# Optimization experiments

Measured on AMD Instinct MI355X. Metric: run time of the kernel, lower is better.

## Reference

```python
import jax, jax.numpy as jnp
import numpy as np

S, R, C, H, D = 128, 384, 256, 8, 32  # N_seq, N_res, C_m, heads, head_dim
INF = 1e9
EPS = 1e-5


def _layernorm(x, w, b):
    mu = jnp.mean(x, axis=-1, keepdims=True)
    var = jnp.mean(jnp.square(x - mu), axis=-1, keepdims=True)
    return (x - mu) * jax.lax.rsqrt(var + EPS) * w + b


def setup_inputs() -> dict:
    key = jax.random.key(0)
    ks = jax.random.split(key, 8)
    sc = 0.02
    m = jax.random.normal(ks[0], (S, R, C), jnp.float32)
    mask = jnp.ones((S, R), jnp.float32)
    ln_w = jnp.ones((C,), jnp.float32)
    ln_b = jnp.zeros((C,), jnp.float32)
    wq = jax.random.normal(ks[1], (C, H * D), jnp.float32) * sc
    wk = jax.random.normal(ks[2], (C, H * D), jnp.float32) * sc
    wv = jax.random.normal(ks[3], (C, H * D), jnp.float32) * sc
    wg = jax.random.normal(ks[4], (C, H * D), jnp.float32) * sc
    bg = jnp.ones((H * D,), jnp.float32)  # gate bias init to 1 (openfold convention)
    wo = jax.random.normal(ks[5], (H * D, C), jnp.float32) * sc
    bo = jnp.zeros((C,), jnp.float32)
    return {"m": m, "mask": mask, "ln_w": ln_w, "ln_b": ln_b,
            "wq": wq, "wk": wk, "wv": wv, "wg": wg, "bg": bg,
            "wo": wo, "bo": bo}


def reference(m, mask, ln_w, ln_b, wq, wk, wv, wg, bg, wo, bo):
    # mask bias: [S, 1, 1, R], 0 where mask==1, -inf-ish where mask==0
    mask_bias = (INF * (mask - 1.0))[:, None, None, :]
    x = _layernorm(m, ln_w, ln_b)                        # [S, R, C]
    q = (x @ wq).reshape(S, R, H, D) * (D ** -0.5)       # [S, R, H, D]
    k = (x @ wk).reshape(S, R, H, D)
    v = (x @ wv).reshape(S, R, H, D)
    scores = jnp.einsum('sqhd,skhd->shqk', q, k) + mask_bias  # [S, H, R, R]
    a = jax.nn.softmax(scores, axis=-1)
    o = jnp.einsum('shqk,skhd->sqhd', a, v)              # [S, R, H, D]
    g = jax.nn.sigmoid(x @ wg + bg).reshape(S, R, H, D)  # gate
    o = (o * g).reshape(S, R, H * D)
    return o @ wo + bo                                   # [S, R, C]
```

## Files before the change

kernel.cpp:

```cpp
#include <hip/hip_runtime.h>
#include <cstdint>
#include <cstddef>

#define S_  128
#define R_  384
#define C_  256
#define H_  8
#define D_  32
#define HD_ 256
#define M_  (S_*R_)

typedef float f32x16 __attribute__((ext_vector_type(16)));
typedef short s16x8  __attribute__((ext_vector_type(8)));
typedef int   i32x4  __attribute__((ext_vector_type(4)));

__device__ __forceinline__ unsigned short f2bf(float f) {
  uint32_t u = __float_as_uint(f);
  u += 0x7fffu + ((u >> 16) & 1u);
  return (unsigned short)(u >> 16);
}
__device__ __forceinline__ float bf2f(unsigned short s) {
  return __uint_as_float(((uint32_t)s) << 16);
}
__device__ __forceinline__ uint32_t pkbf(float lo, float hi) {
  return (uint32_t)f2bf(lo) | ((uint32_t)f2bf(hi) << 16);
}
#define MFMA32(a,b,c) __builtin_amdgcn_mfma_f32_32x32x16_bf16((a),(b),(c),0,0,0)

__global__ __launch_bounds__(256) void prep_w(const float* __restrict__ wq,
    const float* __restrict__ wk, const float* __restrict__ wv,
    const float* __restrict__ wg, const float* __restrict__ wo,
    unsigned short* __restrict__ WT) {
  int idx = blockIdx.x * 256 + threadIdx.x;
  int mat = idx >> 16;
  int rem = idx & 65535;
  int n = rem >> 8, k = rem & 255;
  const float* W = (mat==0)?wq:(mat==1)?wk:(mat==2)?wv:(mat==3)?wg:wo;
  WT[idx] = f2bf(W[k*256 + n]);
}

__global__ __launch_bounds__(256) void ln_kernel(const float* __restrict__ mIn,
    const float* __restrict__ w, const float* __restrict__ b,
    unsigned short* __restrict__ x) {
  int row  = blockIdx.x * 4 + (threadIdx.x >> 6);
  int lane = threadIdx.x & 63;
  const float4 v4 = *(const float4*)(mIn + (size_t)row * C_ + lane * 4);
  float s  = v4.x + v4.y + v4.z + v4.w;
  float ss = v4.x*v4.x + v4.y*v4.y + v4.z*v4.z + v4.w*v4.w;
#pragma unroll
  for (int off = 32; off > 0; off >>= 1) {
    s  += __shfl_xor(s,  off);
    ss += __shfl_xor(ss, off);
  }
  float mu  = s * (1.0f / C_);
  float var = ss * (1.0f / C_) - mu * mu;
  float rs  = rsqrtf(var + 1e-5f);
  const float4 wv = *(const float4*)(w + lane * 4);
  const float4 bv = *(const float4*)(b + lane * 4);
  uint2 o2;
  o2.x = pkbf((v4.x - mu) * rs * wv.x + bv.x, (v4.y - mu) * rs * wv.y + bv.y);
  o2.y = pkbf((v4.z - mu) * rs * wv.z + bv.z, (v4.w - mu) * rs * wv.w + bv.w);
  *(uint2*)(x + (size_t)row * C_ + lane * 4) = o2;
}

__global__ __launch_bounds__(256) void proj_gemm(const unsigned short* __restrict__ X,
    const unsigned short* __restrict__ WT, const float* __restrict__ bg,
    unsigned short* __restrict__ Qo, unsigned short* __restrict__ Ko,
    unsigned short* __restrict__ Vo, unsigned short* __restrict__ Go) {
  __shared__ unsigned short As[128][40];
  __shared__ unsigned short Bs[128][40];
  const int tid = threadIdx.x;
  const int bm  = blockIdx.x * 128;
  const int wi  = blockIdx.y >> 1;
  const int bn  = (blockIdx.y & 1) * 128;
  const unsigned short* Wt = WT + wi * 65536;
  unsigned short* O = (wi==0)?Qo:(wi==1)?Ko:(wi==2)?Vo:Go;

  const int lane = tid & 63, wid = tid >> 6;
  const int wm = (wid >> 1) * 64, wn = (wid & 1) * 64;
  const int lr = lane & 31, hi = lane >> 5;
  const int sr = tid >> 1, sc = (tid & 1) * 16;

  f32x16 acc[2][2];
#pragma unroll
  for (int i = 0; i < 2; i++)
#pragma unroll
    for (int j = 0; j < 2; j++)
#pragma unroll
      for (int r = 0; r < 16; r++) acc[i][j][r] = 0.f;

  for (int k0 = 0; k0 < 256; k0 += 32) {
    const uint4* xs = (const uint4*)(X + (size_t)(bm + sr) * 256 + k0 + sc);
    uint4 x0 = xs[0], x1 = xs[1];
    const uint4* wsrc = (const uint4*)(Wt + (size_t)(bn + sr) * 256 + k0 + sc);
    uint4 b0 = wsrc[0], b1 = wsrc[1];
    *(uint4*)&As[sr][sc] = x0; *(uint4*)&As[sr][sc + 8] = x1;
    *(uint4*)&Bs[sr][sc] = b0; *(uint4*)&Bs[sr][sc + 8] = b1;
    __syncthreads();
#pragma unroll
    for (int kh = 0; kh < 2; kh++) {
      s16x8 a0  = *(const s16x8*)&As[wm + lr][kh*16 + 8*hi];
      s16x8 a1  = *(const s16x8*)&As[wm + 32 + lr][kh*16 + 8*hi];
      s16x8 bb0 = *(const s16x8*)&Bs[wn + lr][kh*16 + 8*hi];
      s16x8 bb1 = *(const s16x8*)&Bs[wn + 32 + lr][kh*16 + 8*hi];
      acc[0][0] = MFMA32(a0, bb0, acc[0][0]);
      acc[0][1] = MFMA32(a0, bb1, acc[0][1]);
      acc[1][0] = MFMA32(a1, bb0, acc[1][0]);
      acc[1][1] = MFMA32(a1, bb1, acc[1][1]);
    }
    __syncthreads();
  }

  const float qs = 0.17677669529663687f;
#pragma unroll
  for (int ms = 0; ms < 2; ms++) {
#pragma unroll
    for (int ns = 0; ns < 2; ns++) {
      int colg = bn + wn + ns*32 + lr;
      float bgv = (wi == 3) ? bg[colg] : 0.f;
#pragma unroll
      for (int r = 0; r < 16; r++) {
        float v = acc[ms][ns][r];
        if (wi == 0) v *= qs;
        if (wi == 3) v = 1.0f / (1.0f + __expf(-(v + bgv)));
        int row = bm + wm + ms*32 + (r & 3) + 8*(r >> 2) + 4*hi;
        O[(size_t)row * 256 + colg] = f2bf(v);
      }
    }
  }
}

__global__ __launch_bounds__(256) void attn_kernel(const unsigned short* __restrict__ Qb,
    const unsigned short* __restrict__ Kb, const unsigned short* __restrict__ Vb,
    const float* __restrict__ mask, unsigned short* __restrict__ Ob) {
  __shared__ unsigned short Kl[384][40];
  __shared__ unsigned short VT[32][392];
  __shared__ float mb[384];
  __shared__ float sAl[4][32];

  const int h = blockIdx.x, s = blockIdx.y;
  const int tid = threadIdx.x;
  const int lane = tid & 63, wid = tid >> 6;
  const int lr = lane & 31, hi = lane >> 5;

#pragma unroll
  for (int i = 0; i < 3; i++) {
    int rh = tid + 256*i;
    int r = rh >> 1, c0 = (rh & 1) * 16;
    const unsigned short* ksrc = Kb + ((size_t)(s*R_ + r)) * 256 + h*32 + c0;
    *(uint4*)&Kl[r][c0]     = *(const uint4*)ksrc;
    *(uint4*)&Kl[r][c0 + 8] = *(const uint4*)(ksrc + 8);
    const unsigned short* vsrc = Vb + ((size_t)(s*R_ + r)) * 256 + h*32 + c0;
    unsigned short tmp[16];
    *(uint4*)tmp       = *(const uint4*)vsrc;
    *(uint4*)(tmp + 8) = *(const uint4*)(vsrc + 8);
#pragma unroll
    for (int j = 0; j < 16; j++) VT[c0 + j][r] = tmp[j];
  }
  for (int r = tid; r < 384; r += 256) mb[r] = 1e9f * (mask[s*R_ + r] - 1.0f);

  s16x8 bq[3][2];
#pragma unroll
  for (int st = 0; st < 3; st++)
#pragma unroll
    for (int kh = 0; kh < 2; kh++)
      bq[st][kh] = *(const s16x8*)(Qb + ((size_t)(s*R_ + wid*96 + st*32 + lr)) * 256
                                   + h*32 + kh*16 + 8*hi);

  f32x16 of[3];
#pragma unroll
  for (int st = 0; st < 3; st++)
#pragma unroll
    for (int r = 0; r < 16; r++) of[st][r] = 0.f;
  float mrun[3] = {-1e30f, -1e30f, -1e30f};
  float lsum[3] = {0.f, 0.f, 0.f};

  __syncthreads();

  for (int kt = 0; kt < 12; kt++) {
    s16x8 ak0 = *(const s16x8*)&Kl[kt*32 + lr][8*hi];
    s16x8 ak1 = *(const s16x8*)&Kl[kt*32 + lr][16 + 8*hi];
    s16x8 bv0 = *(const s16x8*)&VT[lr][kt*32 + 8*hi];
    s16x8 bv1 = *(const s16x8*)&VT[lr][kt*32 + 16 + 8*hi];
    float mbr[16];
#pragma unroll
    for (int r = 0; r < 16; r++) mbr[r] = mb[kt*32 + (r & 3) + 8*(r >> 2) + 4*hi];

#pragma unroll
    for (int st = 0; st < 3; st++) {
      f32x16 p;
#pragma unroll
      for (int r = 0; r < 16; r++) p[r] = 0.f;
      p = MFMA32(ak0, bq[st][0], p);
      p = MFMA32(ak1, bq[st][1], p);
      float pm = -1e30f;
#pragma unroll
      for (int r = 0; r < 16; r++) { p[r] += mbr[r]; pm = fmaxf(pm, p[r]); }
      pm = fmaxf(pm, __shfl_xor(pm, 32));
      if (!__all(pm <= mrun[st] + 8.0f)) {
        float nm = fmaxf(mrun[st], pm);
        float al = __expf(mrun[st] - nm);
        mrun[st] = nm;
        lsum[st] *= al;
        if (hi == 0) sAl[wid][lr] = al;
        float alr[16];
#pragma unroll
        for (int r = 0; r < 16; r++) alr[r] = sAl[wid][(r & 3) + 8*(r >> 2) + 4*hi];
#pragma unroll
        for (int r = 0; r < 16; r++) of[st][r] *= alr[r];
      }
      float ls = 0.f;
#pragma unroll
      for (int r = 0; r < 16; r++) { p[r] = __expf(p[r] - mrun[st]); ls += p[r]; }
      lsum[st] += ls;
      uint32_t w0 = pkbf(p[0],  p[1]),  w1 = pkbf(p[2],  p[3]);
      uint32_t w2 = pkbf(p[4],  p[5]),  w3 = pkbf(p[6],  p[7]);
      uint32_t w4 = pkbf(p[8],  p[9]),  w5 = pkbf(p[10], p[11]);
      uint32_t w6 = pkbf(p[12], p[13]), w7 = pkbf(p[14], p[15]);
      asm volatile("v_permlane32_swap_b32 %0, %1" : "+v"(w0), "+v"(w2));
      asm volatile("v_permlane32_swap_b32 %0, %1" : "+v"(w1), "+v"(w3));
      asm volatile("v_permlane32_swap_b32 %0, %1" : "+v"(w4), "+v"(w6));
      asm volatile("v_permlane32_swap_b32 %0, %1" : "+v"(w5), "+v"(w7));
      i32x4 pa0i = {(int)w0, (int)w1, (int)w2, (int)w3};
      i32x4 pa1i = {(int)w4, (int)w5, (int)w6, (int)w7};
      of[st] = MFMA32(__builtin_bit_cast(s16x8, pa0i), bv0, of[st]);
      of[st] = MFMA32(__builtin_bit_cast(s16x8, pa1i), bv1, of[st]);
    }
  }

#pragma unroll
  for (int st = 0; st < 3; st++) {
    float lt = lsum[st] + __shfl_xor(lsum[st], 32);
    float inv = 1.0f / lt;
    if (hi == 0) sAl[wid][lr] = inv;
    float ivr[16];
#pragma unroll
    for (int r = 0; r < 16; r++) ivr[r] = sAl[wid][(r & 3) + 8*(r >> 2) + 4*hi];
#pragma unroll
    for (int r = 0; r < 16; r++) {
      int row = wid*96 + st*32 + (r & 3) + 8*(r >> 2) + 4*hi;
      Ob[((size_t)(s*R_ + row)) * 256 + h*32 + lr] = f2bf(of[st][r] * ivr[r]);
    }
  }
}

__global__ __launch_bounds__(256) void out_gemm(const unsigned short* __restrict__ Ob,
    const unsigned short* __restrict__ Gb, const unsigned short* __restrict__ WT,
    const float* __restrict__ bo, float* __restrict__ Out) {
  __shared__ unsigned short As[128][40];
  __shared__ unsigned short Bs[128][40];
  const unsigned short* Wt = WT + 4 * 65536;
  const int tid = threadIdx.x;
  const int bm = blockIdx.x * 128;
  const int bn = blockIdx.y * 128;
  const int lane = tid & 63, wid = tid >> 6;
  const int wm = (wid >> 1) * 64, wn = (wid & 1) * 64;
  const int lr = lane & 31, hi = lane >> 5;
  const int sr = tid >> 1, sc = (tid & 1) * 16;

  f32x16 acc[2][2];
#pragma unroll
  for (int i = 0; i < 2; i++)
#pragma unroll
    for (int j = 0; j < 2; j++)
#pragma unroll
      for (int r = 0; r < 16; r++) acc[i][j][r] = 0.f;

  for (int k0 = 0; k0 < 256; k0 += 32) {
    const unsigned short* orow = Ob + (size_t)(bm + sr) * 256 + k0 + sc;
    const unsigned short* grow = Gb + (size_t)(bm + sr) * 256 + k0 + sc;
    unsigned short ot[16], gt[16], res[16];
    *(uint4*)ot       = *(const uint4*)orow;
    *(uint4*)(ot + 8) = *(const uint4*)(orow + 8);
    *(uint4*)gt       = *(const uint4*)grow;
    *(uint4*)(gt + 8) = *(const uint4*)(grow + 8);
#pragma unroll
    for (int j = 0; j < 16; j++) res[j] = f2bf(bf2f(ot[j]) * bf2f(gt[j]));
    const uint4* wsrc = (const uint4*)(Wt + (size_t)(bn + sr) * 256 + k0 + sc);
    uint4 b0 = wsrc[0], b1 = wsrc[1];
    *(uint4*)&As[sr][sc] = *(uint4*)res; *(uint4*)&As[sr][sc + 8] = *(uint4*)(res + 8);
    *(uint4*)&Bs[sr][sc] = b0;           *(uint4*)&Bs[sr][sc + 8] = b1;
    __syncthreads();
#pragma unroll
    for (int kh = 0; kh < 2; kh++) {
      s16x8 a0  = *(const s16x8*)&As[wm + lr][kh*16 + 8*hi];
      s16x8 a1  = *(const s16x8*)&As[wm + 32 + lr][kh*16 + 8*hi];
      s16x8 bb0 = *(const s16x8*)&Bs[wn + lr][kh*16 + 8*hi];
      s16x8 bb1 = *(const s16x8*)&Bs[wn + 32 + lr][kh*16 + 8*hi];
      acc[0][0] = MFMA32(a0, bb0, acc[0][0]);
      acc[0][1] = MFMA32(a0, bb1, acc[0][1]);
      acc[1][0] = MFMA32(a1, bb0, acc[1][0]);
      acc[1][1] = MFMA32(a1, bb1, acc[1][1]);
    }
    __syncthreads();
  }

#pragma unroll
  for (int ms = 0; ms < 2; ms++) {
#pragma unroll
    for (int ns = 0; ns < 2; ns++) {
      int colg = bn + wn + ns*32 + lr;
      float bov = bo[colg];
#pragma unroll
      for (int r = 0; r < 16; r++) {
        int row = bm + wm + ms*32 + (r & 3) + 8*(r >> 2) + 4*hi;
        Out[(size_t)row * 256 + colg] = acc[ms][ns][r] + bov;
      }
    }
  }
}

extern "C" void kernel_launch(void* const* d_in, const int* in_sizes, int n_in,
                              void* d_out, int out_size, void* d_ws, size_t ws_size,
                              hipStream_t stream) {
  const float* m    = (const float*)d_in[0];
  const float* mask = (const float*)d_in[1];
  const float* ln_w = (const float*)d_in[2];
  const float* ln_b = (const float*)d_in[3];
  const float* wq   = (const float*)d_in[4];
  const float* wk   = (const float*)d_in[5];
  const float* wv   = (const float*)d_in[6];
  const float* wg   = (const float*)d_in[7];
  const float* bg   = (const float*)d_in[8];
  const float* wo   = (const float*)d_in[9];
  const float* bo   = (const float*)d_in[10];
  float* out = (float*)d_out;

  unsigned short* ws = (unsigned short*)d_ws;
  const size_t SZ = (size_t)M_ * 256;
  unsigned short* xbf = ws;
  unsigned short* qb  = ws + 1 * SZ;
  unsigned short* kb  = ws + 2 * SZ;
  unsigned short* vb  = ws + 3 * SZ;
  unsigned short* gb  = ws + 4 * SZ;
  unsigned short* ob  = ws + 5 * SZ;
  unsigned short* WT  = ws + 6 * SZ;

  prep_w<<<1280, 256, 0, stream>>>(wq, wk, wv, wg, wo, WT);
  ln_kernel<<<M_ / 4, 256, 0, stream>>>(m, ln_w, ln_b, xbf);
  proj_gemm<<<dim3(M_ / 128, 8), 256, 0, stream>>>(xbf, WT, bg, qb, kb, vb, gb);
  attn_kernel<<<dim3(H_, S_), 256, 0, stream>>>(qb, kb, vb, mask, ob);
  out_gemm<<<dim3(M_ / 128, 2), 256, 0, stream>>>(ob, gb, WT, bo, out);
}
```

Baseline: 270.5 us.

## Use direct global-to-LDS loads, exp2 softmax, gate fusion into attention, tiled weight transpose

The weight-prep kernel now transposes through shared-memory tiles so that both its reads and writes are coalesced. Both GEMMs stage tiles with global_load_lds into unpadded LDS instead of going through registers. Attention folds log2(e) into the Q scale and the mask so the softmax can use exp2. It also loads K/V in two halves to cut LDS use, raises MFMA priority with setprio, and applies the sigmoid gate in its epilogue, so out_gemm no longer reads the gate tensor. The unpadded LDS layout may cause bank conflicts on the MFMA fragment reads.

Result: faster. 262.3 us (-3.0%).

```diff
diff --git a/kernel.cpp b/kernel.cpp
--- a/kernel.cpp
+++ b/kernel.cpp
@@ -10,6 +10,8 @@
 #define HD_ 256
 #define M_  (S_*R_)
 
+#define LOG2E 1.4426950408889634f
+
 typedef float f32x16 __attribute__((ext_vector_type(16)));
 typedef short s16x8  __attribute__((ext_vector_type(8)));
 typedef int   i32x4  __attribute__((ext_vector_type(4)));
@@ -27,16 +29,33 @@
 }
 #define MFMA32(a,b,c) __builtin_amdgcn_mfma_f32_32x32x16_bf16((a),(b),(c),0,0,0)
 
+__device__ __forceinline__ void gload16(const void* g, void* l) {
+  __builtin_amdgcn_global_load_lds(
+      (const __attribute__((address_space(1))) void*)g,
+      (__attribute__((address_space(3))) void*)l, 16, 0, 0);
+}
+
 __global__ __launch_bounds__(256) void prep_w(const float* __restrict__ wq,
     const float* __restrict__ wk, const float* __restrict__ wv,
     const float* __restrict__ wg, const float* __restrict__ wo,
     unsigned short* __restrict__ WT) {
-  int idx = blockIdx.x * 256 + threadIdx.x;
-  int mat = idx >> 16;
-  int rem = idx & 65535;
-  int n = rem >> 8, k = rem & 255;
+  __shared__ unsigned short Tl[64][72];
+  const int mat = blockIdx.x >> 4;
+  const int t   = blockIdx.x & 15;
+  const int k0  = (t >> 2) * 64, n0 = (t & 3) * 64;
   const float* W = (mat==0)?wq:(mat==1)?wk:(mat==2)?wv:(mat==3)?wg:wo;
-  WT[idx] = f2bf(W[k*256 + n]);
+  const int tx = threadIdx.x & 63, ty = threadIdx.x >> 6;
+#pragma unroll
+  for (int i = 0; i < 16; i++) {
+    int kk = ty + i * 4;
+    Tl[tx][kk] = f2bf(W[(size_t)(k0 + kk) * 256 + n0 + tx]);
+  }
+  __syncthreads();
+#pragma unroll
+  for (int i = 0; i < 16; i++) {
+    int nn = ty + i * 4;
+    WT[(size_t)mat * 65536 + (size_t)(n0 + nn) * 256 + k0 + tx] = Tl[nn][tx];
+  }
 }
 
 __global__ __launch_bounds__(256) void ln_kernel(const float* __restrict__ mIn,
@@ -67,19 +86,19 @@
     const unsigned short* __restrict__ WT, const float* __restrict__ bg,
     unsigned short* __restrict__ Qo, unsigned short* __restrict__ Ko,
     unsigned short* __restrict__ Vo, unsigned short* __restrict__ Go) {
-  __shared__ unsigned short As[128][40];
-  __shared__ unsigned short Bs[128][40];
+  __shared__ __align__(16) unsigned short As[128 * 32];
+  __shared__ __align__(16) unsigned short Bs[128 * 32];
   const int tid = threadIdx.x;
   const int bm  = blockIdx.x * 128;
   const int wi  = blockIdx.y >> 1;
   const int bn  = (blockIdx.y & 1) * 128;
-  const unsigned short* Wt = WT + wi * 65536;
+  const unsigned short* Wt = WT + (size_t)wi * 65536;
   unsigned short* O = (wi==0)?Qo:(wi==1)?Ko:(wi==2)?Vo:Go;
 
   const int lane = tid & 63, wid = tid >> 6;
   const int wm = (wid >> 1) * 64, wn = (wid & 1) * 64;
   const int lr = lane & 31, hi = lane >> 5;
-  const int sr = tid >> 1, sc = (tid & 1) * 16;
+  const int srow = lane >> 2, scol = (lane & 3) * 8;
 
   f32x16 acc[2][2];
 #pragma unroll
@@ -90,28 +109,29 @@
       for (int r = 0; r < 16; r++) acc[i][j][r] = 0.f;
 
   for (int k0 = 0; k0 < 256; k0 += 32) {
-    const uint4* xs = (const uint4*)(X + (size_t)(bm + sr) * 256 + k0 + sc);
-    uint4 x0 = xs[0], x1 = xs[1];
-    const uint4* wsrc = (const uint4*)(Wt + (size_t)(bn + sr) * 256 + k0 + sc);
-    uint4 b0 = wsrc[0], b1 = wsrc[1];
-    *(uint4*)&As[sr][sc] = x0; *(uint4*)&As[sr][sc + 8] = x1;
-    *(uint4*)&Bs[sr][sc] = b0; *(uint4*)&Bs[sr][sc + 8] = b1;
+#pragma unroll
+    for (int i = 0; i < 2; i++) {
+      const int rbase = wid * 32 + i * 16;
+      gload16(X  + (size_t)(bm + rbase + srow) * 256 + k0 + scol, &As[rbase * 32]);
+      gload16(Wt + (size_t)(bn + rbase + srow) * 256 + k0 + scol, &Bs[rbase * 32]);
+    }
+    asm volatile("s_waitcnt vmcnt(0)" ::: "memory");
     __syncthreads();
 #pragma unroll
     for (int kh = 0; kh < 2; kh++) {
-      s16x8 a0  = *(const s16x8*)&As[wm + lr][kh*16 + 8*hi];
-      s16x8 a1  = *(const s16x8*)&As[wm + 32 + lr][kh*16 + 8*hi];
-      s16x8 bb0 = *(const s16x8*)&Bs[wn + lr][kh*16 + 8*hi];
-      s16x8 bb1 = *(const s16x8*)&Bs[wn + 32 + lr][kh*16 + 8*hi];
-      acc[0][0] = MFMA32(a0, bb0, acc[0][0]);
-      acc[0][1] = MFMA32(a0, bb1, acc[0][1]);
-      acc[1][0] = MFMA32(a1, bb0, acc[1][0]);
-      acc[1][1] = MFMA32(a1, bb1, acc[1][1]);
-    }
-    __syncthreads();
-  }
-
-  const float qs = 0.17677669529663687f;
+      s16x8 a0 = *(const s16x8*)&As[(wm + lr) * 32      + kh*16 + 8*hi];
+      s16x8 a1 = *(const s16x8*)&As[(wm + 32 + lr) * 32 + kh*16 + 8*hi];
+      s16x8 b0 = *(const s16x8*)&Bs[(wn + lr) * 32      + kh*16 + 8*hi];
+      s16x8 b1 = *(const s16x8*)&Bs[(wn + 32 + lr) * 32 + kh*16 + 8*hi];
+      acc[0][0] = MFMA32(a0, b0, acc[0][0]);
+      acc[0][1] = MFMA32(a0, b1, acc[0][1]);
+      acc[1][0] = MFMA32(a1, b0, acc[1][0]);
+      acc[1][1] = MFMA32(a1, b1, acc[1][1]);
+    }
+    __syncthreads();
+  }
+
+  const float qs2 = 0.17677669529663687f * LOG2E;
 #pragma unroll
   for (int ms = 0; ms < 2; ms++) {
 #pragma unroll
@@ -121,7 +141,7 @@
 #pragma unroll
       for (int r = 0; r < 16; r++) {
         float v = acc[ms][ns][r];
-        if (wi == 0) v *= qs;
+        if (wi == 0) v *= qs2;
         if (wi == 3) v = 1.0f / (1.0f + __expf(-(v + bgv)));
         int row = bm + wm + ms*32 + (r & 3) + 8*(r >> 2) + 4*hi;
         O[(size_t)row * 256 + colg] = f2bf(v);
@@ -132,32 +152,21 @@
 
 __global__ __launch_bounds__(256) void attn_kernel(const unsigned short* __restrict__ Qb,
     const unsigned short* __restrict__ Kb, const unsigned short* __restrict__ Vb,
-    const float* __restrict__ mask, unsigned short* __restrict__ Ob) {
-  __shared__ unsigned short Kl[384][40];
-  __shared__ unsigned short VT[32][392];
+    const unsigned short* __restrict__ Gb, const float* __restrict__ mask,
+    unsigned short* __restrict__ Ob) {
+  __shared__ unsigned short Kl[192][40];
+  __shared__ unsigned short VT[32][200];
   __shared__ float mb[384];
   __shared__ float sAl[4][32];
 
   const int h = blockIdx.x, s = blockIdx.y;
   const int tid = threadIdx.x;
-  const int lane = tid & 63, wid = tid >> 6;
+  const int wid = tid >> 6;
+  const int lane = tid & 63;
   const int lr = lane & 31, hi = lane >> 5;
 
-#pragma unroll
-  for (int i = 0; i < 3; i++) {
-    int rh = tid + 256*i;
-    int r = rh >> 1, c0 = (rh & 1) * 16;
-    const unsigned short* ksrc = Kb + ((size_t)(s*R_ + r)) * 256 + h*32 + c0;
-    *(uint4*)&Kl[r][c0]     = *(const uint4*)ksrc;
-    *(uint4*)&Kl[r][c0 + 8] = *(const uint4*)(ksrc + 8);
-    const unsigned short* vsrc = Vb + ((size_t)(s*R_ + r)) * 256 + h*32 + c0;
-    unsigned short tmp[16];
-    *(uint4*)tmp       = *(const uint4*)vsrc;
-    *(uint4*)(tmp + 8) = *(const uint4*)(vsrc + 8);
-#pragma unroll
-    for (int j = 0; j < 16; j++) VT[c0 + j][r] = tmp[j];
-  }
-  for (int r = tid; r < 384; r += 256) mb[r] = 1e9f * (mask[s*R_ + r] - 1.0f);
+  for (int r = tid; r < 384; r += 256)
+    mb[r] = (1e9f * LOG2E) * (mask[s * R_ + r] - 1.0f);
 
   s16x8 bq[3][2];
 #pragma unroll
@@ -175,56 +184,86 @@
   float mrun[3] = {-1e30f, -1e30f, -1e30f};
   float lsum[3] = {0.f, 0.f, 0.f};
 
-  __syncthreads();
-
-  for (int kt = 0; kt < 12; kt++) {
-    s16x8 ak0 = *(const s16x8*)&Kl[kt*32 + lr][8*hi];
-    s16x8 ak1 = *(const s16x8*)&Kl[kt*32 + lr][16 + 8*hi];
-    s16x8 bv0 = *(const s16x8*)&VT[lr][kt*32 + 8*hi];
-    s16x8 bv1 = *(const s16x8*)&VT[lr][kt*32 + 16 + 8*hi];
-    float mbr[16];
-#pragma unroll
-    for (int r = 0; r < 16; r++) mbr[r] = mb[kt*32 + (r & 3) + 8*(r >> 2) + 4*hi];
-
-#pragma unroll
-    for (int st = 0; st < 3; st++) {
-      f32x16 p;
-#pragma unroll
-      for (int r = 0; r < 16; r++) p[r] = 0.f;
-      p = MFMA32(ak0, bq[st][0], p);
-      p = MFMA32(ak1, bq[st][1], p);
-      float pm = -1e30f;
-#pragma unroll
-      for (int r = 0; r < 16; r++) { p[r] += mbr[r]; pm = fmaxf(pm, p[r]); }
-      pm = fmaxf(pm, __shfl_xor(pm, 32));
-      if (!__all(pm <= mrun[st] + 8.0f)) {
-        float nm = fmaxf(mrun[st], pm);
-        float al = __expf(mrun[st] - nm);
-        mrun[st] = nm;
-        lsum[st] *= al;
-        if (hi == 0) sAl[wid][lr] = al;
-        float alr[16];
-#pragma unroll
-        for (int r = 0; r < 16; r++) alr[r] = sAl[wid][(r & 3) + 8*(r >> 2) + 4*hi];
-#pragma unroll
-        for (int r = 0; r < 16; r++) of[st][r] *= alr[r];
+  for (int ph = 0; ph < 2; ph++) {
+    __syncthreads();
+#pragma unroll
+    for (int i = 0; i < 2; i++) {
+      int rh = tid + 256 * i;
+      if (rh < 384) {
+        int rl = rh >> 1, c0 = (rh & 1) * 16;
+        int rg = ph * 192 + rl;
+        const unsigned short* ksrc = Kb + ((size_t)(s*R_ + rg)) * 256 + h*32 + c0;
+        *(uint4*)&Kl[rl][c0]     = *(const uint4*)ksrc;
+        *(uint4*)&Kl[rl][c0 + 8] = *(const uint4*)(ksrc + 8);
+        const unsigned short* vsrc = Vb + ((size_t)(s*R_ + rg)) * 256 + h*32 + c0;
+        unsigned short tmp[16];
+        *(uint4*)tmp       = *(const uint4*)vsrc;
+        *(uint4*)(tmp + 8) = *(const uint4*)(vsrc + 8);
+#pragma unroll
+        for (int j = 0; j < 16; j++) VT[c0 + j][rl] = tmp[j];
       }
-      float ls = 0.f;
-#pragma unroll
-      for (int r = 0; r < 16; r++) { p[r] = __expf(p[r] - mrun[st]); ls += p[r]; }
-      lsum[st] += ls;
-      uint32_t w0 = pkbf(p[0],  p[1]),  w1 = pkbf(p[2],  p[3]);
-      uint32_t w2 = pkbf(p[4],  p[5]),  w3 = pkbf(p[6],  p[7]);
-      uint32_t w4 = pkbf(p[8],  p[9]),  w5 = pkbf(p[10], p[11]);
-      uint32_t w6 = pkbf(p[12], p[13]), w7 = pkbf(p[14], p[15]);
-      asm volatile("v_permlane32_swap_b32 %0, %1" : "+v"(w0), "+v"(w2));
-      asm volatile("v_permlane32_swap_b32 %0, %1" : "+v"(w1), "+v"(w3));
-      asm volatile("v_permlane32_swap_b32 %0, %1" : "+v"(w4), "+v"(w6));
-      asm volatile("v_permlane32_swap_b32 %0, %1" : "+v"(w5), "+v"(w7));
-      i32x4 pa0i = {(int)w0, (int)w1, (int)w2, (int)w3};
-      i32x4 pa1i = {(int)w4, (int)w5, (int)w6, (int)w7};
-      of[st] = MFMA32(__builtin_bit_cast(s16x8, pa0i), bv0, of[st]);
-      of[st] = MFMA32(__builtin_bit_cast(s16x8, pa1i), bv1, of[st]);
+    }
+    __syncthreads();
+
+    for (int kt = 0; kt < 6; kt++) {
+      const int ktg = ph * 6 + kt;
+      s16x8 ak0 = *(const s16x8*)&Kl[kt*32 + lr][8*hi];
+      s16x8 ak1 = *(const s16x8*)&Kl[kt*32 + lr][16 + 8*hi];
+      s16x8 bv0 = *(const s16x8*)&VT[lr][kt*32 + 8*hi];
+      s16x8 bv1 = *(const s16x8*)&VT[lr][kt*32 + 16 + 8*hi];
+      float mbr[16];
+#pragma unroll
+      for (int r = 0; r < 16; r++) mbr[r] = mb[ktg*32 + (r & 3) + 8*(r >> 2) + 4*hi];
+
+#pragma unroll
+      for (int st = 0; st < 3; st++) {
+        f32x16 p;
+#pragma unroll
+        for (int r = 0; r < 16; r++) p[r] = mbr[r];
+        __builtin_amdgcn_s_setprio(1);
+        p = MFMA32(ak0, bq[st][0], p);
+        p = MFMA32(ak1, bq[st][1], p);
+        __builtin_amdgcn_s_setprio(0);
+        float m01 = fmaxf(fmaxf(p[0], p[1]), fmaxf(p[2], p[3]));
+        float m23 = fmaxf(fmaxf(p[4], p[5]), fmaxf(p[6], p[7]));
+        float m45 = fmaxf(fmaxf(p[8], p[9]), fmaxf(p[10], p[11]));
+        float m67 = fmaxf(fmaxf(p[12], p[13]), fmaxf(p[14], p[15]));
+        float pm = fmaxf(fmaxf(m01, m23), fmaxf(m45, m67));
+        pm = fmaxf(pm, __shfl_xor(pm, 32));
+        if (!__all(pm <= mrun[st] + 11.54f)) {
+          float nm = fmaxf(mrun[st], pm);
+          float al = __builtin_amdgcn_exp2f(mrun[st] - nm);
+          mrun[st] = nm;
+          lsum[st] *= al;
+          if (hi == 0) sAl[wid][lr] = al;
+          float alr[16];
+#pragma unroll
+          for (int r = 0; r < 16; r++) alr[r] = sAl[wid][(r & 3) + 8*(r >> 2) + 4*hi];
+#pragma unroll
+          for (int r = 0; r < 16; r++) of[st][r] *= alr[r];
+        }
+        float ls = 0.f;
+#pragma unroll
+        for (int r = 0; r < 16; r++) {
+          p[r] = __builtin_amdgcn_exp2f(p[r] - mrun[st]);
+          ls += p[r];
+        }
+        lsum[st] += ls;
+        uint32_t w0 = pkbf(p[0],  p[1]),  w1 = pkbf(p[2],  p[3]);
+        uint32_t w2 = pkbf(p[4],  p[5]),  w3 = pkbf(p[6],  p[7]);
+        uint32_t w4 = pkbf(p[8],  p[9]),  w5 = pkbf(p[10], p[11]);
+        uint32_t w6 = pkbf(p[12], p[13]), w7 = pkbf(p[14], p[15]);
+        asm volatile("v_permlane32_swap_b32 %0, %1" : "+v"(w0), "+v"(w2));
+        asm volatile("v_permlane32_swap_b32 %0, %1" : "+v"(w1), "+v"(w3));
+        asm volatile("v_permlane32_swap_b32 %0, %1" : "+v"(w4), "+v"(w6));
+        asm volatile("v_permlane32_swap_b32 %0, %1" : "+v"(w5), "+v"(w7));
+        i32x4 pa0i = {(int)w0, (int)w1, (int)w2, (int)w3};
+        i32x4 pa1i = {(int)w4, (int)w5, (int)w6, (int)w7};
+        __builtin_amdgcn_s_setprio(1);
+        of[st] = MFMA32(__builtin_bit_cast(s16x8, pa0i), bv0, of[st]);
+        of[st] = MFMA32(__builtin_bit_cast(s16x8, pa1i), bv1, of[st]);
+        __builtin_amdgcn_s_setprio(0);
+      }
     }
   }
 
@@ -239,16 +278,18 @@
 #pragma unroll
     for (int r = 0; r < 16; r++) {
       int row = wid*96 + st*32 + (r & 3) + 8*(r >> 2) + 4*hi;
-      Ob[((size_t)(s*R_ + row)) * 256 + h*32 + lr] = f2bf(of[st][r] * ivr[r]);
+      size_t off = ((size_t)(s*R_ + row)) * 256 + h*32 + lr;
+      float gv = bf2f(Gb[off]);
+      Ob[off] = f2bf(of[st][r] * ivr[r] * gv);
     }
   }
 }
 
 __global__ __launch_bounds__(256) void out_gemm(const unsigned short* __restrict__ Ob,
-    const unsigned short* __restrict__ Gb, const unsigned short* __restrict__ WT,
-    const float* __restrict__ bo, float* __restrict__ Out) {
-  __shared__ unsigned short As[128][40];
-  __shared__ unsigned short Bs[128][40];
+    const unsigned short* __restrict__ WT, const float* __restrict__ bo,
+    float* __restrict__ Out) {
+  __shared__ __align__(16) unsigned short As[128 * 32];
+  __shared__ __align__(16) unsigned short Bs[128 * 32];
   const unsigned short* Wt = WT + 4 * 65536;
   const int tid = threadIdx.x;
   const int bm = blockIdx.x * 128;
@@ -256,7 +297,7 @@
   const int lane = tid & 63, wid = tid >> 6;
   const int wm = (wid >> 1) * 64, wn = (wid & 1) * 64;
   const int lr = lane & 31, hi = lane >> 5;
-  const int sr = tid >> 1, sc = (tid & 1) * 16;
+  const int srow = lane >> 2, scol = (lane & 3) * 8;
 
   f32x16 acc[2][2];
 #pragma unroll
@@ -267,30 +308,24 @@
       for (int r = 0; r < 16; r++) acc[i][j][r] = 0.f;
 
   for (int k0 = 0; k0 < 256; k0 += 32) {
-    const unsigned short* orow = Ob + (size_t)(bm + sr) * 256 + k0 + sc;
-    const unsigned short* grow = Gb + (size_t)(bm + sr) * 256 + k0 + sc;
-    unsigned short ot[16], gt[16], res[16];
-    *(uint4*)ot       = *(const uint4*)orow;
-    *(uint4*)(ot + 8) = *(const uint4*)(orow + 8);
-    *(uint4*)gt       = *(const uint4*)grow;
-    *(uint4*)(gt + 8) = *(const uint4*)(grow + 8);
-#pragma unroll
-    for (int j = 0; j < 16; j++) res[j] = f2bf(bf2f(ot[j]) * bf2f(gt[j]));
-    const uint4* wsrc = (const uint4*)(Wt + (size_t)(bn + sr) * 256 + k0 + sc);
-    uint4 b0 = wsrc[0], b1 = wsrc[1];
-    *(uint4*)&As[sr][sc] = *(uint4*)res; *(uint4*)&As[sr][sc + 8] = *(uint4*)(res + 8);
-    *(uint4*)&Bs[sr][sc] = b0;           *(uint4*)&Bs[sr][sc + 8] = b1;
+#pragma unroll
+    for (int i = 0; i < 2; i++) {
+      const int rbase = wid * 32 + i * 16;
+      gload16(Ob + (size_t)(bm + rbase + srow) * 256 + k0 + scol, &As[rbase * 32]);
+      gload16(Wt + (size_t)(bn + rbase + srow) * 256 + k0 + scol, &Bs[rbase * 32]);
+    }
+    asm volatile("s_waitcnt vmcnt(0)" ::: "memory");
     __syncthreads();
 #pragma unroll
     for (int kh = 0; kh < 2; kh++) {
-      s16x8 a0  = *(const s16x8*)&As[wm + lr][kh*16 + 8*hi];
-      s16x8 a1  = *(const s16x8*)&As[wm + 32 + lr][kh*16 + 8*hi];
-      s16x8 bb0 = *(const s16x8*)&Bs[wn + lr][kh*16 + 8*hi];
-      s16x8 bb1 = *(const s16x8*)&Bs[wn + 32 + lr][kh*16 + 8*hi];
-      acc[0][0] = MFMA32(a0, bb0, acc[0][0]);
-      acc[0][1] = MFMA32(a0, bb1, acc[0][1]);
-      acc[1][0] = MFMA32(a1, bb0, acc[1][0]);
-      acc[1][1] = MFMA32(a1, bb1, acc[1][1]);
+      s16x8 a0 = *(const s16x8*)&As[(wm + lr) * 32      + kh*16 + 8*hi];
+      s16x8 a1 = *(const s16x8*)&As[(wm + 32 + lr) * 32 + kh*16 + 8*hi];
+      s16x8 b0 = *(const s16x8*)&Bs[(wn + lr) * 32      + kh*16 + 8*hi];
+      s16x8 b1 = *(const s16x8*)&Bs[(wn + 32 + lr) * 32 + kh*16 + 8*hi];
+      acc[0][0] = MFMA32(a0, b0, acc[0][0]);
+      acc[0][1] = MFMA32(a0, b1, acc[0][1]);
+      acc[1][0] = MFMA32(a1, b0, acc[1][0]);
+      acc[1][1] = MFMA32(a1, b1, acc[1][1]);
     }
     __syncthreads();
   }
@@ -336,9 +371,9 @@
   unsigned short* ob  = ws + 5 * SZ;
   unsigned short* WT  = ws + 6 * SZ;
 
-  prep_w<<<1280, 256, 0, stream>>>(wq, wk, wv, wg, wo, WT);
+  prep_w<<<80, 256, 0, stream>>>(wq, wk, wv, wg, wo, WT);
   ln_kernel<<<M_ / 4, 256, 0, stream>>>(m, ln_w, ln_b, xbf);
   proj_gemm<<<dim3(M_ / 128, 8), 256, 0, stream>>>(xbf, WT, bg, qb, kb, vb, gb);
-  attn_kernel<<<dim3(H_, S_), 256, 0, stream>>>(qb, kb, vb, mask, ob);
-  out_gemm<<<dim3(M_ / 128, 2), 256, 0, stream>>>(ob, gb, WT, bo, out);
-}
+  attn_kernel<<<dim3(H_, S_), 256, 0, stream>>>(qb, kb, vb, gb, mask, ob);
+  out_gemm<<<dim3(M_ / 128, 2), 256, 0, stream>>>(ob, WT, bo, out);
+}
```
